# Performance work log

Measured on AMD Instinct MI355X. Metric: run time of the kernel, lower is better.

The kernel has to match this reference:

```python
import jax, jax.numpy as jnp
import numpy as np
from jax import lax


def _fps(xyz, num_group):
    """Farthest point sampling. xyz: (B, N, 3) -> centers (B, G, 3).
    Sequential over G (structural loop) via lax.scan; starts at index 0."""
    B, N, _ = xyz.shape

    def step(carry, _):
        min_d, last_idx = carry                      # (B, N), (B,)
        last_pt = jax.vmap(lambda p, i: p[i])(xyz, last_idx)  # (B, 3)
        d = jnp.sum((xyz - last_pt[:, None, :]) ** 2, axis=-1)  # (B, N)
        min_d = jnp.minimum(min_d, d)
        nxt = jnp.argmax(min_d, axis=-1).astype(jnp.int32)
        return (min_d, nxt), last_idx

    init = (jnp.full((B, N), jnp.inf, dtype=xyz.dtype),
            jnp.zeros((B,), dtype=jnp.int32))
    _, idxs = lax.scan(step, init, None, length=num_group)  # (G, B)
    idxs = idxs.T                                            # (B, G)
    centers = jax.vmap(lambda p, i: p[i])(xyz, idxs)         # (B, G, 3)
    return centers


def setup_inputs() -> dict:
    key = jax.random.key(0)
    xyz = jax.random.normal(key, (32, 8192, 3), dtype=jnp.float32)
    return {"xyz": xyz, "num_group": 256, "group_size": 32}


def reference(xyz, num_group, group_size):
    B, N, C = xyz.shape
    center = _fps(xyz, num_group)                            # (B, G, 3)
    # dense pairwise distances: (B, G, N)
    dist = jnp.linalg.norm(center[:, :, None, :] - xyz[:, None, :, :], axis=-1)
    _, idx = lax.top_k(-dist, group_size)                    # (B, G, k) smallest dists
    # gather neighbors per batch: (B, G, k, 3)
    patch = jax.vmap(lambda pts, i: pts[i])(xyz, idx)
    patch = patch - center[:, :, None, :]                    # recenter
    return (patch, center)
```

## Files before the change

kernel.cpp:

```cpp
#include <hip/hip_runtime.h>

#pragma clang fp contract(off)

#define BB 32
#define NN 8192
#define GG 256
#define KK 32

#define TFPS 512
#define JPF (NN / TFPS)

template <int CTRL>
__device__ __forceinline__ float dppmax_f(float v) {
  const int o =
      __builtin_amdgcn_update_dpp(0, __float_as_int(v), CTRL, 0xF, 0xF, true);
  return fmaxf(v, __int_as_float(o));
}

template <int CTRL>
__device__ __forceinline__ unsigned dppmax_u(unsigned v) {
  const unsigned o =
      (unsigned)__builtin_amdgcn_update_dpp(0, (int)v, CTRL, 0xF, 0xF, true);
  return o > v ? o : v;
}

__global__ __launch_bounds__(TFPS, 1) void fps_kernel(const float* __restrict__ xyz,
                                                      float* __restrict__ out) {
#pragma clang fp contract(off)
  const int b = blockIdx.x;
  const int t = threadIdx.x;
  const int lane = t & 63;
  const int wave = t >> 6;
  const float* __restrict__ P = xyz + (size_t)b * NN * 3;

  __shared__ float4 pts[NN];
  __shared__ unsigned long long warr[2][8];

  float px[JPF], py[JPF], pz[JPF], md[JPF];
#pragma unroll
  for (int j = 0; j < JPF; ++j) {
    const int idx = t + j * TFPS;
    const float x = P[idx * 3 + 0];
    const float y = P[idx * 3 + 1];
    const float z = P[idx * 3 + 2];
    px[j] = x; py[j] = y; pz[j] = z;
    md[j] = __builtin_inff();
    pts[idx] = make_float4(x, y, z, 0.0f);
  }
  __syncthreads();

  unsigned win = 0;
  unsigned mywin = 0;

  for (int i = 0; i < GG; ++i) {
    if (t == i) mywin = win;
    if (i == GG - 1) break;

    const float4 c = pts[win];
    const float cx = c.x, cy = c.y, cz = c.z;

    float bv = -1.0f;
#pragma unroll
    for (int j = 0; j < JPF; ++j) {
      const float dx = px[j] - cx;
      const float dy = py[j] - cy;
      const float dz = pz[j] - cz;
      const float d = dx * dx + dy * dy + dz * dz;
      const float m = md[j] < d ? md[j] : d;
      md[j] = m;
      bv = fmaxf(bv, m);
    }

    float v = bv;
    v = dppmax_f<0x121>(v);
    v = dppmax_f<0x122>(v);
    v = dppmax_f<0x124>(v);
    v = dppmax_f<0x128>(v);
    v = dppmax_f<0x142>(v);
    v = dppmax_f<0x143>(v);
    const unsigned Mw =
        (unsigned)__builtin_amdgcn_readlane(__float_as_int(v), 63);

    unsigned cbi = 0u;
    if (__float_as_uint(bv) == Mw) {
      int fj = 0;
#pragma unroll
      for (int j = JPF - 1; j >= 0; --j)
        if (__float_as_uint(md[j]) == Mw) fj = j;
      cbi = ~((unsigned)t + ((unsigned)fj << 9));
    }
    cbi = dppmax_u<0x121>(cbi);
    cbi = dppmax_u<0x122>(cbi);
    cbi = dppmax_u<0x124>(cbi);
    cbi = dppmax_u<0x128>(cbi);
    cbi = dppmax_u<0x142>(cbi);
    cbi = dppmax_u<0x143>(cbi);

    if (lane == 63)
      warr[i & 1][wave] = ((unsigned long long)Mw << 32) | cbi;
    __syncthreads();

    const unsigned long long* __restrict__ w = warr[i & 1];
    unsigned long long best = w[0];
#pragma unroll
    for (int k = 1; k < 8; ++k) {
      const unsigned long long e = w[k];
      best = e > best ? e : best;
    }
    win = ~(unsigned)best;
  }

  if (t < GG) {
    const float4 c = pts[mywin];
    float* __restrict__ co =
        out + (size_t)BB * GG * KK * 3 + ((size_t)b * GG + t) * 3;
    co[0] = c.x; co[1] = c.y; co[2] = c.z;
  }
}

__global__ __launch_bounds__(512, 1) void knn_kernel(const float* __restrict__ xyz,
                                                     float* __restrict__ out) {
#pragma clang fp contract(off)
  const int b = blockIdx.x >> 3;
  const int chunk = blockIdx.x & 7;
  const int t = threadIdx.x;
  const int lane = t & 63;
  const int wave = t >> 6;
  const float* __restrict__ P = xyz + (size_t)b * NN * 3;

  __shared__ float xs[NN], ys[NN], zs[NN];
  __shared__ unsigned long long cand[8][256];

  for (int pt = t; pt < NN; pt += 512) {
    xs[pt] = P[pt * 3 + 0];
    ys[pt] = P[pt * 3 + 1];
    zs[pt] = P[pt * 3 + 2];
  }
  __syncthreads();

  const float* __restrict__ cent = out + (size_t)BB * GG * KK * 3;

  for (int gi = 0; gi < 4; ++gi) {
    const int g = chunk * 32 + wave * 4 + gi;
    const float cx = cent[((size_t)b * GG + g) * 3 + 0];
    const float cy = cent[((size_t)b * GG + g) * 3 + 1];
    const float cz = cent[((size_t)b * GG + g) * 3 + 2];

    float d2r[128];
    float mn = __builtin_inff();
#pragma unroll
    for (int j = 0; j < 128; ++j) {
      const int idx = lane + j * 64;
      const float dx = xs[idx] - cx;
      const float dy = ys[idx] - cy;
      const float dz = zs[idx] - cz;
      const float d2 = dx * dx + dy * dy + dz * dz;
      d2r[j] = d2;
      mn = fminf(mn, d2);
    }

    float sm = mn;
#pragma unroll
    for (int k = 2; k <= 64; k <<= 1) {
#pragma unroll
      for (int j2 = k >> 1; j2 > 0; j2 >>= 1) {
        const float o = __shfl_xor(sm, j2, 64);
        const bool keepMin = (((lane & k) == 0) == ((lane & j2) == 0));
        sm = keepMin ? fminf(sm, o) : fmaxf(sm, o);
      }
    }
    const float v = __shfl(sm, 31, 64);
    const float vi = __uint_as_float(__float_as_uint(v) + 8);

    unsigned cnt = 0;
    unsigned long long* __restrict__ cb = cand[wave];
#pragma unroll
    for (int j = 0; j < 128; ++j) {
      const bool p = d2r[j] <= vi;
      const unsigned long long mk = __ballot(p);
      if (p) {
        const unsigned off = cnt + (unsigned)__popcll(mk & ((1ull << lane) - 1));
        if (off < 256)
          cb[off] = ((unsigned long long)__float_as_uint(d2r[j]) << 32) |
                    (unsigned)(lane + j * 64);
      }
      cnt += (unsigned)__popcll(mk);
    }
    if (cnt > 256) cnt = 256;

    auto conv = [](unsigned long long e) -> unsigned long long {
      const float d = sqrtf(__uint_as_float((unsigned)(e >> 32)));
      return ((unsigned long long)__float_as_uint(d) << 32) | (e & 0xFFFFFFFFull);
    };

    unsigned long long myk;
    if (cnt <= 64) {
      unsigned long long key = ~0ull;
      if ((unsigned)lane < cnt) key = conv(cb[lane]);
#pragma unroll
      for (int k = 2; k <= 64; k <<= 1) {
#pragma unroll
        for (int j2 = k >> 1; j2 > 0; j2 >>= 1) {
          const unsigned long long o = __shfl_xor(key, j2, 64);
          const bool keepMin = (((lane & k) == 0) == ((lane & j2) == 0));
          const unsigned long long lo = o < key ? o : key;
          const unsigned long long hi = o < key ? key : o;
          key = keepMin ? lo : hi;
        }
      }
      myk = key;
    } else {
      unsigned long long k0 = ~0ull, k1 = ~0ull, k2 = ~0ull, k3 = ~0ull;
      if ((unsigned)lane < cnt)         k0 = conv(cb[lane]);
      if ((unsigned)(lane + 64) < cnt)  k1 = conv(cb[lane + 64]);
      if ((unsigned)(lane + 128) < cnt) k2 = conv(cb[lane + 128]);
      if ((unsigned)(lane + 192) < cnt) k3 = conv(cb[lane + 192]);
      unsigned long long got = ~0ull;
      for (int r = 0; r < 32; ++r) {
        unsigned long long m01 = k0 < k1 ? k0 : k1;
        unsigned long long m23 = k2 < k3 ? k2 : k3;
        unsigned long long m = m01 < m23 ? m01 : m23;
#pragma unroll
        for (int s = 32; s > 0; s >>= 1) {
          const unsigned long long o = __shfl_xor(m, s, 64);
          m = o < m ? o : m;
        }
        if (lane == r) got = m;
        if (k0 == m) k0 = ~0ull;
        else if (k1 == m) k1 = ~0ull;
        else if (k2 == m) k2 = ~0ull;
        else if (k3 == m) k3 = ~0ull;
      }
      myk = got;
    }

    if (lane < KK) {
      const unsigned idx = (unsigned)(myk & 0xFFFFFFFFull);
      const float ox = xs[idx] - cx;
      const float oy = ys[idx] - cy;
      const float oz = zs[idx] - cz;
      float* __restrict__ po = out + ((size_t)(((size_t)b * GG + g) * KK + lane)) * 3;
      po[0] = ox; po[1] = oy; po[2] = oz;
    }
  }
}

extern "C" void kernel_launch(void* const* d_in, const int* in_sizes, int n_in,
                              void* d_out, int out_size, void* d_ws, size_t ws_size,
                              hipStream_t stream) {
  const float* xyz = (const float*)d_in[0];
  float* out = (float*)d_out;
  fps_kernel<<<dim3(BB), dim3(TFPS), 0, stream>>>(xyz, out);
  knn_kernel<<<dim3(BB * 8), dim3(512), 0, stream>>>(xyz, out);
}
```

Before: 343.3 us.

## Broadcast FPS winner coordinates via shared slots; recompute kNN distances instead of caching

```diff
diff --git a/kernel.cpp b/kernel.cpp
--- a/kernel.cpp
+++ b/kernel.cpp
@@ -33,32 +33,24 @@
   const int wave = t >> 6;
   const float* __restrict__ P = xyz + (size_t)b * NN * 3;
 
-  __shared__ float4 pts[NN];
-  __shared__ unsigned long long warr[2][8];
+  __shared__ unsigned long long skey[2][8];
+  __shared__ float4 scrd[2][8];
 
   float px[JPF], py[JPF], pz[JPF], md[JPF];
 #pragma unroll
   for (int j = 0; j < JPF; ++j) {
     const int idx = t + j * TFPS;
-    const float x = P[idx * 3 + 0];
-    const float y = P[idx * 3 + 1];
-    const float z = P[idx * 3 + 2];
-    px[j] = x; py[j] = y; pz[j] = z;
+    px[j] = P[idx * 3 + 0];
+    py[j] = P[idx * 3 + 1];
+    pz[j] = P[idx * 3 + 2];
     md[j] = __builtin_inff();
-    pts[idx] = make_float4(x, y, z, 0.0f);
-  }
-  __syncthreads();
-
-  unsigned win = 0;
-  unsigned mywin = 0;
-
-  for (int i = 0; i < GG; ++i) {
-    if (t == i) mywin = win;
-    if (i == GG - 1) break;
-
-    const float4 c = pts[win];
-    const float cx = c.x, cy = c.y, cz = c.z;
-
+  }
+
+  float cx = P[0], cy = P[1], cz = P[2];
+  float sx = 0.f, sy = 0.f, sz = 0.f;
+  if (t == 0) { sx = cx; sy = cy; sz = cz; }
+
+  for (int i = 0; i < GG - 1; ++i) {
     float bv = -1.0f;
 #pragma unroll
     for (int j = 0; j < JPF; ++j) {
@@ -81,40 +73,47 @@
     const unsigned Mw =
         (unsigned)__builtin_amdgcn_readlane(__float_as_int(v), 63);
 
-    unsigned cbi = 0u;
-    if (__float_as_uint(bv) == Mw) {
-      int fj = 0;
-#pragma unroll
-      for (int j = JPF - 1; j >= 0; --j)
-        if (__float_as_uint(md[j]) == Mw) fj = j;
-      cbi = ~((unsigned)t + ((unsigned)fj << 9));
-    }
-    cbi = dppmax_u<0x121>(cbi);
-    cbi = dppmax_u<0x122>(cbi);
-    cbi = dppmax_u<0x124>(cbi);
-    cbi = dppmax_u<0x128>(cbi);
-    cbi = dppmax_u<0x142>(cbi);
-    cbi = dppmax_u<0x143>(cbi);
-
-    if (lane == 63)
-      warr[i & 1][wave] = ((unsigned long long)Mw << 32) | cbi;
+    int fj = 0;
+#pragma unroll
+    for (int j = JPF - 1; j >= 0; --j)
+      if (__float_as_uint(md[j]) == Mw) fj = j;
+    const unsigned cbi = (__float_as_uint(bv) == Mw)
+                             ? ~((unsigned)t + ((unsigned)fj << 9))
+                             : 0u;
+
+    unsigned r = cbi;
+    r = dppmax_u<0x121>(r);
+    r = dppmax_u<0x122>(r);
+    r = dppmax_u<0x124>(r);
+    r = dppmax_u<0x128>(r);
+    r = dppmax_u<0x142>(r);
+    r = dppmax_u<0x143>(r);
+    const unsigned wIdx = (unsigned)__builtin_amdgcn_readlane((int)r, 63);
+
+    if (cbi == wIdx) {
+      skey[i & 1][wave] = ((unsigned long long)Mw << 32) | wIdx;
+      scrd[i & 1][wave] = make_float4(px[fj], py[fj], pz[fj], 0.f);
+    }
     __syncthreads();
 
-    const unsigned long long* __restrict__ w = warr[i & 1];
-    unsigned long long best = w[0];
+    const unsigned long long* __restrict__ kk = skey[i & 1];
+    const float4* __restrict__ cc = scrd[i & 1];
+    unsigned long long bk = kk[0];
+    float4 bc = cc[0];
 #pragma unroll
     for (int k = 1; k < 8; ++k) {
-      const unsigned long long e = w[k];
-      best = e > best ? e : best;
-    }
-    win = ~(unsigned)best;
+      const unsigned long long e = kk[k];
+      const float4 ec = cc[k];
+      if (e > bk) { bk = e; bc = ec; }
+    }
+    cx = bc.x; cy = bc.y; cz = bc.z;
+    if (t == i + 1) { sx = cx; sy = cy; sz = cz; }
   }
 
   if (t < GG) {
-    const float4 c = pts[mywin];
     float* __restrict__ co =
         out + (size_t)BB * GG * KK * 3 + ((size_t)b * GG + t) * 3;
-    co[0] = c.x; co[1] = c.y; co[2] = c.z;
+    co[0] = sx; co[1] = sy; co[2] = sz;
   }
 }
 
@@ -146,16 +145,14 @@
     const float cy = cent[((size_t)b * GG + g) * 3 + 1];
     const float cz = cent[((size_t)b * GG + g) * 3 + 2];
 
-    float d2r[128];
     float mn = __builtin_inff();
-#pragma unroll
+#pragma unroll 8
     for (int j = 0; j < 128; ++j) {
       const int idx = lane + j * 64;
       const float dx = xs[idx] - cx;
       const float dy = ys[idx] - cy;
       const float dz = zs[idx] - cz;
       const float d2 = dx * dx + dy * dy + dz * dz;
-      d2r[j] = d2;
       mn = fminf(mn, d2);
     }
 
@@ -174,15 +171,20 @@
 
     unsigned cnt = 0;
     unsigned long long* __restrict__ cb = cand[wave];
-#pragma unroll
+#pragma unroll 8
     for (int j = 0; j < 128; ++j) {
-      const bool p = d2r[j] <= vi;
+      const int idx = lane + j * 64;
+      const float dx = xs[idx] - cx;
+      const float dy = ys[idx] - cy;
+      const float dz = zs[idx] - cz;
+      const float d2 = dx * dx + dy * dy + dz * dz;
+      const bool p = d2 <= vi;
       const unsigned long long mk = __ballot(p);
       if (p) {
         const unsigned off = cnt + (unsigned)__popcll(mk & ((1ull << lane) - 1));
         if (off < 256)
-          cb[off] = ((unsigned long long)__float_as_uint(d2r[j]) << 32) |
-                    (unsigned)(lane + j * 64);
+          cb[off] = ((unsigned long long)__float_as_uint(d2) << 32) |
+                    (unsigned)idx;
       }
       cnt += (unsigned)__popcll(mk);
     }
```

New measurement: 527.4 us. 53.6% more time.
